# Optimization experiments

Measured on AMD Instinct MI355X. Metric: run time of the kernel, lower is better.

## Reference

```python
import jax, jax.numpy as jnp
import numpy as np

B, C_IN, C_OUT, H, MAXN = 128, 32, 32, 4096, 6


def setup_inputs() -> dict:
    key = jax.random.key(0)
    ks = jax.random.split(key, 6)
    x = jax.random.normal(ks[0], (B, C_IN, H), dtype=jnp.float32)
    weight = jax.random.normal(ks[1], (C_OUT, C_IN, MAXN + 1), dtype=jnp.float32) * 0.05
    bias = jax.random.normal(ks[2], (C_OUT,), dtype=jnp.float32) * 0.05
    gamma = jnp.ones((C_OUT,), dtype=jnp.float32)
    beta = jnp.zeros((C_OUT,), dtype=jnp.float32)
    # hex neighbor table; -1 marks invalid (boundary) neighbors
    neighbors = jax.random.randint(ks[3], (H, MAXN), -1, H, dtype=jnp.int64)
    return {"x": x, "weight": weight, "bias": bias, "gamma": gamma,
            "beta": beta, "neighbors": neighbors, "groups": 1}


def reference(x, weight, bias, gamma, beta, neighbors, groups):
    Bsz, Cin, Hn = x.shape
    Cout, _, K = weight.shape  # K = total_inputs = max_neighbors + 1
    G = groups
    # global std normalization (torch std: unbiased, ddof=1)
    x = x / (jnp.std(x, ddof=1) + 1e-5)
    valid = (neighbors >= 0)                      # [H, K-1]
    idx = jnp.clip(neighbors, 0, None)
    nbr = x[:, :, idx] * valid.astype(x.dtype)[None, None]   # [B,C,H,K-1]
    allv = jnp.concatenate([x[..., None], nbr], axis=3)      # [B,C,H,K]
    allv = allv.reshape(Bsz, G, Cin // G, Hn, K)
    w = weight.reshape(G, Cout // G, Cin // G, K)
    out = jnp.einsum('bgihk,goik->bgoh', allv, w).reshape(Bsz, Cout, Hn)
    total_valid = valid.sum(axis=1).astype(out.dtype)[None, None] + 1.0  # [1,1,H]
    out = out / (total_valid + 1e-6)
    out = out + bias[None, :, None]
    # BatchNorm1d in training mode: per-channel over (batch, hex), biased var
    mean = out.mean(axis=(0, 2), keepdims=True)
    var = out.var(axis=(0, 2), keepdims=True)
    out = gamma[None, :, None] * (out - mean) * jax.lax.rsqrt(var + 1e-5) + beta[None, :, None]
    return out
```

## Files before the change

### kernel.cpp

```cpp
#include <hip/hip_runtime.h>
#include <stdint.h>
#include <stddef.h>

#define BSZ 128
#define CIN 32
#define COUT 32
#define HN 4096
#define K7 7
#define NTOT (BSZ*CIN*HN)
#define NBH  (BSZ*HN)

typedef __attribute__((ext_vector_type(8))) short short8;
typedef __attribute__((ext_vector_type(4))) float f32x4;

#define WS_OB   0
#define WS_WT   33554432
#define WS_NBR  33568768
#define WS_INVD 33699840
#define WS_OSTP 33716224
#define WS_OST  33781760

__device__ __forceinline__ unsigned short f32_to_bf16(float f){
    union { float f; uint32_t u; } v; v.f = f;
    uint32_t u = v.u;
    return (unsigned short)((u + 0x7FFFu + ((u >> 16) & 1u)) >> 16);
}
__device__ __forceinline__ float bf16_to_f32(unsigned short h){
    union { uint32_t u; float f; } v; v.u = ((uint32_t)h) << 16;
    return v.f;
}

__global__ void ktrans(const float* __restrict__ x,
                       unsigned short* __restrict__ xt,
                       const int* __restrict__ nbr,
                       const float* __restrict__ w,
                       int* __restrict__ nbr_pack,
                       float* __restrict__ invd,
                       unsigned short* __restrict__ wt,
                       float* __restrict__ ostatp){
    __shared__ float tile[32][260];
    int b  = blockIdx.x >> 4;
    int h0 = (blockIdx.x & 15) << 8;
    int t  = threadIdx.x;
    #pragma unroll
    for (int l = 0; l < 8; l++){
        int linear = l*256 + t;
        int c  = linear >> 6;
        int h4 = linear & 63;
        float4 v = *(const float4*)(x + ((size_t)(b*CIN + c))*HN + h0 + h4*4);
        *(float4*)&tile[c][h4*4] = v;
    }
    __syncthreads();
    int cg = (t & 3) * 8;
    int hw = t >> 2;
    #pragma unroll
    for (int r = 0; r < 4; r++){
        int h = r*64 + hw;
        alignas(16) unsigned short tmp[8];
        #pragma unroll
        for (int j = 0; j < 8; j++) tmp[j] = f32_to_bf16(tile[cg + j][h]);
        *(uint4*)(xt + ((size_t)(b*HN + h0 + h))*32 + cg) = *(const uint4*)tmp;
    }
    if (blockIdx.x < 16){
        int h = blockIdx.x*256 + t;
        #pragma unroll
        for (int j = 0; j < 4; j++) ostatp[h*4 + j] = 0.0f;
        int cnt = 0;
        int pk[8];
        #pragma unroll
        for (int j = 0; j < 6; j++){
            int iv = nbr[h*6 + j];
            if (iv >= HN) iv = HN - 1;
            if (iv >= 0) cnt++; else iv = -1;
            pk[j] = iv;
        }
        pk[6] = cnt; pk[7] = 0;
        #pragma unroll
        for (int j = 0; j < 8; j++) nbr_pack[h*8 + j] = pk[j];
        invd[h] = 1.0f / ((float)cnt + 1.0f + 1e-6f);
    } else if (blockIdx.x == 16){
        for (int i = t; i < COUT*K7*CIN; i += 256){
            int o  = i / (K7*CIN);
            int kk = (i / CIN) % K7;
            int c  = i % CIN;
            wt[i] = f32_to_bf16(w[(o*CIN + c)*K7 + kk]);
        }
    }
}

__global__ __launch_bounds__(256) void kconv(
    const unsigned short* __restrict__ xt,
    const unsigned short* __restrict__ wt,
    const int* __restrict__ nbrp,
    const float* __restrict__ invd,
    unsigned short* __restrict__ ob,
    float* __restrict__ ostatp)
{
    __shared__ unsigned short otile[4][32][72];

    int lane = threadIdx.x & 63;
    int wv   = threadIdx.x >> 6;
    int n    = lane & 15;
    int quad = lane >> 4;
    int xcd  = blockIdx.x & 7;
    int j    = blockIdx.x >> 3;
    int b    = xcd*16 + (j >> 4);
    int hbase= ((j & 15)*4 + wv) * 64;

    short8 af[2][K7];
    #pragma unroll
    for (int mt = 0; mt < 2; mt++){
        int o = n + 16*mt;
        #pragma unroll
        for (int kk = 0; kk < K7; kk++)
            af[mt][kk] = *(const short8*)(wt + (size_t)(o*K7 + kk)*CIN + quad*8);
    }

    float sacc[8]  = {0,0,0,0,0,0,0,0};
    float sacc2[8] = {0,0,0,0,0,0,0,0};
    const short8 zero8 = {0,0,0,0,0,0,0,0};
    const unsigned short* xb = xt + (size_t)b*HN*CIN;

    int h = hbase + n;
    int4 na = *(const int4*)(nbrp + h*8);
    int4 nb = *(const int4*)(nbrp + h*8 + 4);
    float idv = invd[h];

    #pragma unroll 1
    for (int it = 0; it < 4; it++){
        int hn = hbase + (it < 3 ? it+1 : it)*16 + n;
        int4 na2 = *(const int4*)(nbrp + hn*8);
        int4 nb2 = *(const int4*)(nbrp + hn*8 + 4);
        float idv2 = invd[hn];

        int hc = hbase + it*16 + n;
        short8 bfr[K7];
        bfr[0] = *(const short8*)(xb + (size_t)hc*CIN + quad*8);
        int rows[6] = {na.x, na.y, na.z, na.w, nb.x, nb.y};
        #pragma unroll
        for (int kk = 0; kk < 6; kk++){
            int row  = rows[kk];
            int rowc = row < 0 ? 0 : row;
            bfr[kk+1] = *(const short8*)(xb + (size_t)rowc*CIN + quad*8);
            if (row < 0) bfr[kk+1] = zero8;
        }
        f32x4 acc0 = {0.f,0.f,0.f,0.f};
        f32x4 acc1 = {0.f,0.f,0.f,0.f};
        #pragma unroll
        for (int kk = 0; kk < K7; kk++){
            acc0 = __builtin_amdgcn_mfma_f32_16x16x32_bf16(af[0][kk], bfr[kk], acc0, 0, 0, 0);
            acc1 = __builtin_amdgcn_mfma_f32_16x16x32_bf16(af[1][kk], bfr[kk], acc1, 0, 0, 0);
        }
        #pragma unroll
        for (int mt = 0; mt < 2; mt++){
            f32x4 a = mt ? acc1 : acc0;
            #pragma unroll
            for (int r = 0; r < 4; r++){
                int o = mt*16 + quad*4 + r;
                float v = a[r]*idv;
                otile[wv][o][it*16 + n] = f32_to_bf16(v);
                sacc[mt*4 + r]  += v;
                sacc2[mt*4 + r] += v*v;
            }
        }
        na = na2; nb = nb2; idv = idv2;
    }

    #pragma unroll
    for (int ro = 0; ro < 4; ro++){
        int o  = ro*8 + (lane >> 3);
        int hh = (lane & 7)*8;
        uint4 vv = *(const uint4*)&otile[wv][o][hh];
        *(uint4*)(ob + ((size_t)(b*COUT + o))*HN + hbase + hh) = vv;
    }

    #pragma unroll
    for (int bit = 1; bit < 16; bit <<= 1){
        #pragma unroll
        for (int i = 0; i < 8; i++){
            sacc[i]  += __shfl_xor(sacc[i],  bit);
            sacc2[i] += __shfl_xor(sacc2[i], bit);
        }
    }
    if (n == 0){
        int slot = blockIdx.x & 255;
        #pragma unroll
        for (int mt = 0; mt < 2; mt++)
            #pragma unroll
            for (int r = 0; r < 4; r++){
                int o = mt*16 + quad*4 + r;
                atomicAdd(&ostatp[slot*64 + o],      sacc[mt*4 + r]);
                atomicAdd(&ostatp[slot*64 + 32 + o], sacc2[mt*4 + r]);
            }
    }
}

__global__ void kred(const float* __restrict__ ostatp,
                     float* __restrict__ ostat){
    __shared__ float part[4][64];
    int t = threadIdx.x;
    int a = t & 63;
    int g = t >> 6;
    float s = 0.0f;
    #pragma unroll
    for (int j = 0; j < 64; j++)
        s += ostatp[(g*64 + j)*64 + a];
    part[g][a] = s;
    __syncthreads();
    if (t < 64)
        ostat[t] = part[0][t] + part[1][t] + part[2][t] + part[3][t];
}

__global__ void kbn(const unsigned short* __restrict__ ob,
                    float* __restrict__ out,
                    const float* __restrict__ ostat,
                    const float* __restrict__ gamma,
                    const float* __restrict__ beta){
    __shared__ float sc[32], sh[32];
    int t = threadIdx.x;
    if (t < 32){
        float mean = ostat[t] * (1.0f/(float)NBH);
        float var  = ostat[32 + t] * (1.0f/(float)NBH) - mean*mean;
        float s = gamma[t] * rsqrtf(var + 1e-5f);
        sc[t] = s;
        sh[t] = beta[t] - mean*s;
    }
    __syncthreads();
    int gid    = blockIdx.x*blockDim.x + t;
    int stride = gridDim.x*blockDim.x;
    for (int i = gid; i < NTOT/8; i += stride){
        int o = (i >> 9) & 31;
        uint4 raw = ((const uint4*)ob)[i];
        const unsigned short* p = (const unsigned short*)&raw;
        float s = sc[o], bsh = sh[o];
        float4 r0, r1;
        r0.x = bf16_to_f32(p[0])*s + bsh;
        r0.y = bf16_to_f32(p[1])*s + bsh;
        r0.z = bf16_to_f32(p[2])*s + bsh;
        r0.w = bf16_to_f32(p[3])*s + bsh;
        r1.x = bf16_to_f32(p[4])*s + bsh;
        r1.y = bf16_to_f32(p[5])*s + bsh;
        r1.z = bf16_to_f32(p[6])*s + bsh;
        r1.w = bf16_to_f32(p[7])*s + bsh;
        ((float4*)out)[i*2]     = r0;
        ((float4*)out)[i*2 + 1] = r1;
    }
}

extern "C" void kernel_launch(void* const* d_in, const int* in_sizes, int n_in,
                              void* d_out, int out_size, void* d_ws, size_t ws_size,
                              hipStream_t stream) {
    const float* x      = (const float*)d_in[0];
    const float* weight = (const float*)d_in[1];
    const float* gamma  = (const float*)d_in[3];
    const float* beta   = (const float*)d_in[4];
    const int*   nbr    = (const int*)d_in[5];

    char* ws = (char*)d_ws;
    unsigned short* ob    = (unsigned short*)(ws + WS_OB);
    unsigned short* wt    = (unsigned short*)(ws + WS_WT);
    int*            nbrp  = (int*)(ws + WS_NBR);
    float*          invd  = (float*)(ws + WS_INVD);
    float*          ostatp= (float*)(ws + WS_OSTP);
    float*          ostat = (float*)(ws + WS_OST);
    float*          out   = (float*)d_out;
    unsigned short* xt    = (unsigned short*)d_out + 16777216;

    ktrans<<<2048, 256, 0, stream>>>(x, xt, nbr, weight, nbrp, invd, wt, ostatp);
    kconv <<<2048, 256, 0, stream>>>(xt, wt, nbrp, invd, ob, ostatp);
    kred  <<<1,    256, 0, stream>>>(ostatp, ostat);
    kbn   <<<2048, 256, 0, stream>>>(ob, out, ostat, gamma, beta);
}
```

Measured before the change: 175.3 us.

## Fold BN stat reduction into conv via last-block counter, add nontemporal memory ops

Measured after the change: 256.4 us. 1.46x slower.

```diff
diff --git a/kernel.cpp b/kernel.cpp
--- a/kernel.cpp
+++ b/kernel.cpp
@@ -12,6 +12,8 @@
 
 typedef __attribute__((ext_vector_type(8))) short short8;
 typedef __attribute__((ext_vector_type(4))) float f32x4;
+typedef __attribute__((ext_vector_type(4))) unsigned int u32x4;
+typedef __attribute__((ext_vector_type(2))) unsigned int u32x2;
 
 #define WS_OB   0
 #define WS_WT   33554432
@@ -19,6 +21,7 @@
 #define WS_INVD 33699840
 #define WS_OSTP 33716224
 #define WS_OST  33781760
+#define WS_CTR  33782016
 
 __device__ __forceinline__ unsigned short f32_to_bf16(float f){
     union { float f; uint32_t u; } v; v.f = f;
@@ -37,7 +40,8 @@
                        int* __restrict__ nbr_pack,
                        float* __restrict__ invd,
                        unsigned short* __restrict__ wt,
-                       float* __restrict__ ostatp){
+                       float* __restrict__ ostatp,
+                       unsigned int* __restrict__ ctr){
     __shared__ float tile[32][260];
     int b  = blockIdx.x >> 4;
     int h0 = (blockIdx.x & 15) << 8;
@@ -47,8 +51,9 @@
         int linear = l*256 + t;
         int c  = linear >> 6;
         int h4 = linear & 63;
-        float4 v = *(const float4*)(x + ((size_t)(b*CIN + c))*HN + h0 + h4*4);
-        *(float4*)&tile[c][h4*4] = v;
+        f32x4 v = __builtin_nontemporal_load(
+            (const f32x4*)(x + ((size_t)(b*CIN + c))*HN + h0 + h4*4));
+        *(f32x4*)&tile[c][h4*4] = v;
     }
     __syncthreads();
     int cg = (t & 3) * 8;
@@ -59,7 +64,8 @@
         alignas(16) unsigned short tmp[8];
         #pragma unroll
         for (int j = 0; j < 8; j++) tmp[j] = f32_to_bf16(tile[cg + j][h]);
-        *(uint4*)(xt + ((size_t)(b*HN + h0 + h))*32 + cg) = *(const uint4*)tmp;
+        __builtin_nontemporal_store(*(const u32x4*)tmp,
+            (u32x4*)(xt + ((size_t)(b*HN + h0 + h))*32 + cg));
     }
     if (blockIdx.x < 16){
         int h = blockIdx.x*256 + t;
@@ -79,6 +85,7 @@
         for (int j = 0; j < 8; j++) nbr_pack[h*8 + j] = pk[j];
         invd[h] = 1.0f / ((float)cnt + 1.0f + 1e-6f);
     } else if (blockIdx.x == 16){
+        if (t == 0) *ctr = 0u;
         for (int i = t; i < COUT*K7*CIN; i += 256){
             int o  = i / (K7*CIN);
             int kk = (i / CIN) % K7;
@@ -94,9 +101,15 @@
     const int* __restrict__ nbrp,
     const float* __restrict__ invd,
     unsigned short* __restrict__ ob,
-    float* __restrict__ ostatp)
+    float* __restrict__ ostatp,
+    float* __restrict__ ostat,
+    const float* __restrict__ gamma,
+    const float* __restrict__ beta,
+    unsigned int* __restrict__ ctr)
 {
     __shared__ unsigned short otile[4][32][72];
+    __shared__ float rpart[4][64];
+    __shared__ int slast;
 
     int lane = threadIdx.x & 63;
     int wv   = threadIdx.x >> 6;
@@ -170,8 +183,9 @@
     for (int ro = 0; ro < 4; ro++){
         int o  = ro*8 + (lane >> 3);
         int hh = (lane & 7)*8;
-        uint4 vv = *(const uint4*)&otile[wv][o][hh];
-        *(uint4*)(ob + ((size_t)(b*COUT + o))*HN + hbase + hh) = vv;
+        u32x4 vv = *(const u32x4*)&otile[wv][o][hh];
+        __builtin_nontemporal_store(vv,
+            (u32x4*)(ob + ((size_t)(b*COUT + o))*HN + hbase + hh));
     }
 
     #pragma unroll
@@ -193,57 +207,60 @@
                 atomicAdd(&ostatp[slot*64 + 32 + o], sacc2[mt*4 + r]);
             }
     }
-}
-
-__global__ void kred(const float* __restrict__ ostatp,
-                     float* __restrict__ ostat){
-    __shared__ float part[4][64];
-    int t = threadIdx.x;
-    int a = t & 63;
-    int g = t >> 6;
-    float s = 0.0f;
-    #pragma unroll
-    for (int j = 0; j < 64; j++)
-        s += ostatp[(g*64 + j)*64 + a];
-    part[g][a] = s;
-    __syncthreads();
-    if (t < 64)
-        ostat[t] = part[0][t] + part[1][t] + part[2][t] + part[3][t];
+
+    __syncthreads();
+    if (threadIdx.x == 0){
+        __threadfence();
+        unsigned d = atomicAdd(ctr, 1u);
+        slast = (d == 2047u);
+    }
+    __syncthreads();
+    if (!slast) return;
+    {
+        int t = threadIdx.x;
+        int a = t & 63, g = t >> 6;
+        float s = 0.0f;
+        #pragma unroll
+        for (int jj = 0; jj < 64; jj++)
+            s += ostatp[((g << 6) + jj)*64 + a];
+        rpart[g][a] = s;
+        __syncthreads();
+        if (t < 64)
+            rpart[0][t] = rpart[0][t] + rpart[1][t] + rpart[2][t] + rpart[3][t];
+        __syncthreads();
+        if (t < 32){
+            float mean = rpart[0][t]      * (1.0f/(float)NBH);
+            float var  = rpart[0][32 + t] * (1.0f/(float)NBH) - mean*mean;
+            float sc = gamma[t] * rsqrtf(var + 1e-5f);
+            ostat[t]      = sc;
+            ostat[32 + t] = beta[t] - mean*sc;
+        }
+    }
 }
 
 __global__ void kbn(const unsigned short* __restrict__ ob,
                     float* __restrict__ out,
-                    const float* __restrict__ ostat,
-                    const float* __restrict__ gamma,
-                    const float* __restrict__ beta){
+                    const float* __restrict__ ostat){
     __shared__ float sc[32], sh[32];
     int t = threadIdx.x;
-    if (t < 32){
-        float mean = ostat[t] * (1.0f/(float)NBH);
-        float var  = ostat[32 + t] * (1.0f/(float)NBH) - mean*mean;
-        float s = gamma[t] * rsqrtf(var + 1e-5f);
-        sc[t] = s;
-        sh[t] = beta[t] - mean*s;
-    }
-    __syncthreads();
-    int gid    = blockIdx.x*blockDim.x + t;
-    int stride = gridDim.x*blockDim.x;
-    for (int i = gid; i < NTOT/8; i += stride){
-        int o = (i >> 9) & 31;
-        uint4 raw = ((const uint4*)ob)[i];
+    if (t < 32){ sc[t] = ostat[t]; sh[t] = ostat[32 + t]; }
+    __syncthreads();
+    int gid = blockIdx.x*256 + t;
+    const u32x2* ob2 = (const u32x2*)ob;
+    f32x4* out4 = (f32x4*)out;
+    #pragma unroll
+    for (int k = 0; k < 8; k++){
+        int i = gid + k*(2048*256);
+        int o = (i >> 10) & 31;
+        u32x2 raw = __builtin_nontemporal_load(ob2 + i);
         const unsigned short* p = (const unsigned short*)&raw;
         float s = sc[o], bsh = sh[o];
-        float4 r0, r1;
-        r0.x = bf16_to_f32(p[0])*s + bsh;
-        r0.y = bf16_to_f32(p[1])*s + bsh;
-        r0.z = bf16_to_f32(p[2])*s + bsh;
-        r0.w = bf16_to_f32(p[3])*s + bsh;
-        r1.x = bf16_to_f32(p[4])*s + bsh;
-        r1.y = bf16_to_f32(p[5])*s + bsh;
-        r1.z = bf16_to_f32(p[6])*s + bsh;
-        r1.w = bf16_to_f32(p[7])*s + bsh;
-        ((float4*)out)[i*2]     = r0;
-        ((float4*)out)[i*2 + 1] = r1;
+        f32x4 r;
+        r.x = bf16_to_f32(p[0])*s + bsh;
+        r.y = bf16_to_f32(p[1])*s + bsh;
+        r.z = bf16_to_f32(p[2])*s + bsh;
+        r.w = bf16_to_f32(p[3])*s + bsh;
+        __builtin_nontemporal_store(r, out4 + i);
     }
 }
 
@@ -263,11 +280,11 @@
     float*          invd  = (float*)(ws + WS_INVD);
     float*          ostatp= (float*)(ws + WS_OSTP);
     float*          ostat = (float*)(ws + WS_OST);
+    unsigned int*   ctr   = (unsigned int*)(ws + WS_CTR);
     float*          out   = (float*)d_out;
     unsigned short* xt    = (unsigned short*)d_out + 16777216;
 
-    ktrans<<<2048, 256, 0, stream>>>(x, xt, nbr, weight, nbrp, invd, wt, ostatp);
-    kconv <<<2048, 256, 0, stream>>>(xt, wt, nbrp, invd, ob, ostatp);
-    kred  <<<1,    256, 0, stream>>>(ostatp, ostat);
-    kbn   <<<2048, 256, 0, stream>>>(ob, out, ostat, gamma, beta);
-}
+    ktrans<<<2048, 256, 0, stream>>>(x, xt, nbr, weight, nbrp, invd, wt, ostatp, ctr);
+    kconv <<<2048, 256, 0, stream>>>(xt, wt, nbrp, invd, ob, ostatp, ostat, gamma, beta, ctr);
+    kbn   <<<2048, 256, 0, stream>>>(ob, out, ostat);
+}
```
